# Kernel tuning notes

Hardware: AMD Instinct MI355X
Metric: run time of the kernel (lower is better)

The kernel has to match this reference:

```python
import jax, jax.numpy as jnp
import numpy as np

N = 100000      # nodes
NT = 500000     # unique (s,o) pairs
R = 16          # original relations
RP = 16         # latent relations
EMB = 16
NUMCLS = 40


def setup_inputs() -> dict:
    key = jax.random.key(0)
    ks = jax.random.split(key, 10)
    s = jax.random.randint(ks[0], (NT,), 0, N)
    o = jax.random.randint(ks[1], (NT,), 0, N)
    rm = jnp.arange(RP)
    # faithful to source: oe = o*rm, se = s*rm (values in [0, N*RP))
    hrow = jnp.broadcast_to(s[None, :], (RP, NT)).reshape(-1).astype(jnp.int64)
    hcol = (o[None, :] * rm[:, None]).reshape(-1).astype(jnp.int64)
    vrow = (s[None, :] * rm[:, None]).reshape(-1).astype(jnp.int64)
    vcol = jnp.broadcast_to(o[None, :], (RP, NT)).reshape(-1).astype(jnp.int64)
    # multi-hot relation indicators per unique pair
    nhots = (jax.random.uniform(ks[2], (NT, R)) < 0.15).astype(jnp.float32)
    xav = lambda k, shp, fan: (jax.random.normal(k, shp, jnp.float32) * np.sqrt(2.0 / fan)).astype(jnp.float32)
    return {
        'nhots': nhots,
        'Wl1': xav(ks[3], (RP, R), R), 'bl1': jnp.zeros((RP,), jnp.float32),
        'Wl2': xav(ks[4], (RP, R), R), 'bl2': jnp.zeros((RP,), jnp.float32),
        'weights1': xav(ks[5], (RP, N, EMB), N),
        'weights2': xav(ks[6], (RP, EMB, NUMCLS), EMB),
        'bias1': jnp.zeros((EMB,), jnp.float32),
        'bias2': jnp.zeros((NUMCLS,), jnp.float32),
        'hrow': hrow, 'hcol': hcol, 'vrow': vrow, 'vcol': vcol,
    }


def reference(nhots, Wl1, bl1, Wl2, bl2, weights1, weights2, bias1, bias2,
              hrow, hcol, vrow, vcol):
    rp, n, e = weights1.shape
    nrp = n * rp
    # --- layer 1: softmax-gated latent relation values, column-normalized ---
    lat1 = jax.nn.softmax(nhots @ Wl1.T + bl1, axis=1)          # (nt, rp)
    vals1 = lat1.T.reshape(-1)                                   # (rp*nt,) rp-major, matches index order
    colsum = jax.ops.segment_sum(vals1, hcol, num_segments=nrp)
    vals1 = vals1 / colsum[hcol]
    # spmm: (n, n*rp) sparse  x  (n*rp, e) dense
    wflat = weights1.reshape(nrp, e)
    h = jax.ops.segment_sum(vals1[:, None] * wflat[hcol], hrow, num_segments=n)  # (n, e)
    h = jax.nn.relu(h + bias1)
    # --- layer 2: row-normalized ---
    lat2 = jax.nn.softmax(nhots @ Wl2.T + bl2, axis=1)
    vals2 = lat2.T.reshape(-1)
    rowsum = jax.ops.segment_sum(vals2, vrow, num_segments=nrp)
    vals2 = vals2 / rowsum[vrow]
    # spmm: (n*rp, n) sparse  x  (n, e) dense
    h2 = jax.ops.segment_sum(vals2[:, None] * h[vcol], vrow, num_segments=nrp)   # (n*rp, e)
    h2 = h2.reshape(rp, n, e)
    out = jnp.einsum('rhc,rnh->nc', weights2, h2) + bias2        # (n, numcls)
    return out
```

## Files before the change

### kernel.cpp

```cpp
#include <hip/hip_runtime.h>
#include <stdint.h>

#define NN 100000
#define NT 500000
#define RP 16
#define RR 16
#define EMB 16
#define NUMCLS 40
#define NRP (NN*RP)
#define MM (2*NN)
#define SCAN_BLOCKS ((MM + 255)/256)
#define NB16 6250

__global__ __launch_bounds__(256) void k_count(const int* __restrict__ s,
                                               const int* __restrict__ o,
                                               int* __restrict__ cnt){
    int t = blockIdx.x*256 + threadIdx.x;
    if (t >= NT) return;
    atomicAdd(&cnt[s[t]], 1);
    atomicAdd(&cnt[NN + o[t]], 1);
}

__global__ __launch_bounds__(256) void k_scan_blk(const int* __restrict__ cnt,
                                                  int* __restrict__ offs,
                                                  int* __restrict__ bsum){
    __shared__ int sm[256];
    int tid = threadIdx.x;
    int i = blockIdx.x*256 + tid;
    int v = (i < MM) ? cnt[i] : 0;
    sm[tid] = v; __syncthreads();
    for (int off = 1; off < 256; off <<= 1){
        int x = (tid >= off) ? sm[tid-off] : 0;
        __syncthreads();
        sm[tid] += x; __syncthreads();
    }
    if (i < MM) offs[i] = sm[tid] - v;
    if (tid == 255) bsum[blockIdx.x] = sm[255];
}

__global__ __launch_bounds__(1024) void k_scan_top(const int* __restrict__ bsum,
                                                   int* __restrict__ btot){
    __shared__ int sm[1024];
    int tid = threadIdx.x;
    int v = (tid < SCAN_BLOCKS) ? bsum[tid] : 0;
    sm[tid] = v; __syncthreads();
    for (int off = 1; off < 1024; off <<= 1){
        int x = (tid >= off) ? sm[tid-off] : 0;
        __syncthreads();
        sm[tid] += x; __syncthreads();
    }
    if (tid < SCAN_BLOCKS) btot[tid] = sm[tid] - v;
}

__global__ __launch_bounds__(256) void k_scan_add(int* __restrict__ offs,
                                                  const int* __restrict__ btot,
                                                  int* __restrict__ cur){
    int i = blockIdx.x*256 + threadIdx.x;
    if (i < MM){
        int v = offs[i] + btot[blockIdx.x];
        offs[i] = v;
        cur[i] = v;
    }
    if (i == 0) offs[MM] = 2*NT;
}

__global__ __launch_bounds__(256) void k_lat(
    const float* __restrict__ nhots,
    const float* __restrict__ Wl1, const float* __restrict__ bl1,
    const float* __restrict__ Wl2, const float* __restrict__ bl2,
    const int* __restrict__ srow, const int* __restrict__ ocol,
    int* __restrict__ cur,
    float* __restrict__ lat1q, float* __restrict__ lat2p,
    int* __restrict__ o_at_p, int* __restrict__ s_at_q)
{
    __shared__ float sW1[RP*RR], sW2[RP*RR], sb1[RP], sb2[RP];
    __shared__ float st1[256][17], st2[256][17];
    __shared__ int sq[256], sp[256];
    int tid = threadIdx.x;
    if (tid < RP*RR){ sW1[tid] = Wl1[tid]; sW2[tid] = Wl2[tid]; }
    if (tid < RP){ sb1[tid] = bl1[tid]; sb2[tid] = bl2[tid]; }
    __syncthreads();

    int t = blockIdx.x*256 + tid;
    int p = -1, q = -1;
    if (t < NT){
        int s_ = srow[t], o_ = ocol[t];
        p = atomicAdd(&cur[s_], 1);
        q = atomicAdd(&cur[NN + o_], 1) - NT;
        o_at_p[p] = o_;
        s_at_q[q] = s_;

        float nh[RR];
        const float4* npx = (const float4*)(nhots + (size_t)t * RR);
        #pragma unroll
        for (int u = 0; u < 4; u++){
            float4 v = npx[u];
            nh[4*u] = v.x; nh[4*u+1] = v.y; nh[4*u+2] = v.z; nh[4*u+3] = v.w;
        }
        float l1[RP], l2[RP];
        #pragma unroll
        for (int r = 0; r < RP; r++){
            float a = sb1[r], b = sb2[r];
            #pragma unroll
            for (int i = 0; i < RR; i++){ a += nh[i]*sW1[r*RR+i]; b += nh[i]*sW2[r*RR+i]; }
            l1[r] = a; l2[r] = b;
        }
        float m1 = l1[0], m2 = l2[0];
        #pragma unroll
        for (int r = 1; r < RP; r++){ m1 = fmaxf(m1, l1[r]); m2 = fmaxf(m2, l2[r]); }
        float s1 = 0.f, s2 = 0.f;
        #pragma unroll
        for (int r = 0; r < RP; r++){
            l1[r] = expf(l1[r]-m1); s1 += l1[r];
            l2[r] = expf(l2[r]-m2); s2 += l2[r];
        }
        float i1 = 1.f/s1, i2 = 1.f/s2;
        #pragma unroll
        for (int r = 0; r < RP; r++){ st1[tid][r] = l1[r]*i1; st2[tid][r] = l2[r]*i2; }
    }
    sq[tid] = q; sp[tid] = p;
    __syncthreads();

    int g = tid >> 4, e = tid & 15;
    #pragma unroll
    for (int k = 0; k < 16; k++){
        int ei = k*16 + g;
        int qq = sq[ei];
        if (qq >= 0){
            lat1q[(size_t)qq*16 + e] = st1[ei][e];
            lat2p[(size_t)sp[ei]*16 + e] = st2[ei][e];
        }
    }
}

__global__ __launch_bounds__(256) void k_CR(const int* __restrict__ offs,
                                            const float* __restrict__ lat1q,
                                            const float* __restrict__ lat2p,
                                            float* __restrict__ C,
                                            float* __restrict__ Rm,
                                            float* __restrict__ pbC,
                                            float* __restrict__ pbR){
    int gid = blockIdx.x*256 + threadIdx.x;
    int n = gid >> 4, e = gid & 15;
    float accC = 0.f, accR = 0.f;
    if (n < NN){
        int b = offs[NN+n] - NT, en = offs[NN+n+1] - NT;
        for (int i = b; i < en; i++) accC += lat1q[(size_t)i*16 + e];
        C[(size_t)n*16 + e] = accC;
        b = offs[n]; en = offs[n+1];
        for (int i = b; i < en; i++) accR += lat2p[(size_t)i*16 + e];
        Rm[(size_t)n*16 + e] = accR;
    }
    __shared__ float sa[16], sb[16];
    int g = threadIdx.x >> 4;
    if (e == 0){ sa[g] = accC; sb[g] = accR; }
    __syncthreads();
    if (threadIdx.x == 0){
        float a = 0.f, b = 0.f;
        #pragma unroll
        for (int k = 0; k < 16; k++){ a += sa[k]; b += sb[k]; }
        pbC[blockIdx.x] = a;
        pbR[blockIdx.x] = b;
    }
}

__global__ __launch_bounds__(1024) void k_red1(const float* __restrict__ pbC,
                                               const float* __restrict__ pbR,
                                               float* __restrict__ S0V){
    __shared__ float sa[1024], sb[1024];
    int tid = threadIdx.x;
    float a = 0.f, b = 0.f;
    for (int i = tid; i < NB16; i += 1024){ a += pbC[i]; b += pbR[i]; }
    sa[tid] = a; sb[tid] = b; __syncthreads();
    for (int off = 512; off > 0; off >>= 1){
        if (tid < off){ sa[tid] += sa[tid+off]; sb[tid] += sb[tid+off]; }
        __syncthreads();
    }
    if (tid == 0){ S0V[0] = sa[0]; S0V[1] = sb[0]; }
}

__global__ __launch_bounds__(256) void k_sums(const float* __restrict__ C,
                                              const float* __restrict__ Rm,
                                              const float* __restrict__ S0,
                                              float* __restrict__ invc,
                                              float* __restrict__ invr){
    int c = blockIdx.x*256 + threadIdx.x;
    if (c >= NRP) return;
    float a = 0.f, b = 0.f;
    if (c == 0){ a = S0[0]; b = S0[1]; }
    #pragma unroll
    for (int r = 1; r < RP; r++){
        int q = c / r;
        if (q*r == c && q < NN){
            a += C[(size_t)q*16 + r];
            b += Rm[(size_t)q*16 + r];
        }
    }
    invc[c] = (a > 0.f) ? 1.f/a : 0.f;
    invr[c] = (b > 0.f) ? 1.f/b : 0.f;
}

__global__ __launch_bounds__(256) void k_y(const int* __restrict__ offs,
                                           const float* __restrict__ lat1q,
                                           const int* __restrict__ s_at_q,
                                           const float* __restrict__ invc,
                                           const float* __restrict__ w1,
                                           float* __restrict__ hsum){
    int gid = blockIdx.x*256 + threadIdx.x;
    int o = gid >> 4, e = gid & 15;
    if (o >= NN) return;
    float Wb[RP];
    #pragma unroll
    for (int r = 0; r < RP; r++){
        size_t c = (size_t)o * r;
        Wb[r] = invc[c] * w1[c*16 + e];
    }
    int b = offs[NN+o] - NT, en = offs[NN+o+1] - NT;
    for (int i = b; i < en; i++){
        const float4* lp = (const float4*)(lat1q + (size_t)i*16);
        float4 v0 = lp[0], v1 = lp[1], v2 = lp[2], v3 = lp[3];
        float y = v0.x*Wb[0] + v0.y*Wb[1] + v0.z*Wb[2] + v0.w*Wb[3]
                + v1.x*Wb[4] + v1.y*Wb[5] + v1.z*Wb[6] + v1.w*Wb[7]
                + v2.x*Wb[8] + v2.y*Wb[9] + v2.z*Wb[10]+ v2.w*Wb[11]
                + v3.x*Wb[12]+ v3.y*Wb[13]+ v3.z*Wb[14]+ v3.w*Wb[15];
        int s = s_at_q[i];
        unsafeAtomicAdd(&hsum[(size_t)s*16 + e], y);
    }
}

__global__ __launch_bounds__(256) void k_P(const int* __restrict__ offs,
                                           const int* __restrict__ o_at_p,
                                           const float* __restrict__ lat2p,
                                           const float* __restrict__ hsum,
                                           const float* __restrict__ b1,
                                           float* __restrict__ P,
                                           float* __restrict__ pbV){
    int gid = blockIdx.x*256 + threadIdx.x;
    int n = gid >> 4, e = gid & 15;
    float be = b1[e];
    float acc[RP];
    #pragma unroll
    for (int r = 0; r < RP; r++) acc[r] = 0.f;
    if (n < NN){
        int b = offs[n], en = offs[n+1];
        for (int i = b; i < en; i++){
            int o = o_at_p[i];
            float hv = fmaxf(hsum[(size_t)o*16 + e] + be, 0.f);
            const float4* lp = (const float4*)(lat2p + (size_t)i*16);
            float4 v0 = lp[0], v1 = lp[1], v2 = lp[2], v3 = lp[3];
            acc[0] += v0.x*hv; acc[1] += v0.y*hv; acc[2] += v0.z*hv; acc[3] += v0.w*hv;
            acc[4] += v1.x*hv; acc[5] += v1.y*hv; acc[6] += v1.z*hv; acc[7] += v1.w*hv;
            acc[8] += v2.x*hv; acc[9] += v2.y*hv; acc[10]+= v2.z*hv; acc[11]+= v2.w*hv;
            acc[12]+= v3.x*hv; acc[13]+= v3.y*hv; acc[14]+= v3.z*hv; acc[15]+= v3.w*hv;
        }
        float* Pn = P + (size_t)n*240 + e;
        #pragma unroll
        for (int r = 1; r < RP; r++) Pn[(r-1)*16] = acc[r];
    }
    __shared__ float sm[256];
    sm[threadIdx.x] = acc[0]; __syncthreads();
    if (threadIdx.x < 16){
        float s = 0.f;
        #pragma unroll
        for (int k = 0; k < 16; k++) s += sm[k*16 + threadIdx.x];
        pbV[(size_t)blockIdx.x*16 + threadIdx.x] = s;
    }
}

__global__ __launch_bounds__(256) void k_red2(const float* __restrict__ pbV,
                                              float* __restrict__ S0V){
    int e = blockIdx.x;
    __shared__ float sm[256];
    int tid = threadIdx.x;
    float a = 0.f;
    for (int i = tid; i < NB16; i += 256) a += pbV[(size_t)i*16 + e];
    sm[tid] = a; __syncthreads();
    for (int off = 128; off > 0; off >>= 1){
        if (tid < off) sm[tid] += sm[tid+off];
        __syncthreads();
    }
    if (tid == 0) S0V[2 + e] = sm[0];
}

__global__ __launch_bounds__(256) void k_out(const float* __restrict__ P,
                                             const float* __restrict__ invr,
                                             const float* __restrict__ S0V,
                                             const float* __restrict__ w2,
                                             const float* __restrict__ b2,
                                             float* __restrict__ out){
    __shared__ float sm[4][64][41];
    int tid = threadIdx.x;
    int w = tid >> 6;
    int lane = tid & 63;
    int n = blockIdx.x*64 + lane;
    float acc[NUMCLS];
    #pragma unroll
    for (int cl = 0; cl < NUMCLS; cl++) acc[cl] = 0.f;
    if (n < NN){
        #pragma unroll 1
        for (int rw = 0; rw < 4; rw++){
            int rr = w + rw*4;
            int c = rr*NN + n;
            float hrow[EMB];
            #pragma unroll
            for (int e = 0; e < EMB; e++) hrow[e] = 0.f;
            if (c == 0){
                #pragma unroll
                for (int e = 0; e < EMB; e++) hrow[e] = S0V[2+e];
            }
            #pragma unroll
            for (int r = 1; r < RP; r++){
                int q = c / r;
                if (q*r == c && q < NN){
                    const float4* Pr = (const float4*)(P + (size_t)q*240 + (r-1)*16);
                    float4 a0 = Pr[0], a1 = Pr[1], a2 = Pr[2], a3 = Pr[3];
                    hrow[0]+=a0.x;  hrow[1]+=a0.y;  hrow[2]+=a0.z;  hrow[3]+=a0.w;
                    hrow[4]+=a1.x;  hrow[5]+=a1.y;  hrow[6]+=a1.z;  hrow[7]+=a1.w;
                    hrow[8]+=a2.x;  hrow[9]+=a2.y;  hrow[10]+=a2.z; hrow[11]+=a2.w;
                    hrow[12]+=a3.x; hrow[13]+=a3.y; hrow[14]+=a3.z; hrow[15]+=a3.w;
                }
            }
            float inv = invr[c];
            const float* wr = w2 + (size_t)rr*EMB*NUMCLS;
            #pragma unroll
            for (int e = 0; e < EMB; e++){
                float x = hrow[e] * inv;
                #pragma unroll
                for (int cl = 0; cl < NUMCLS; cl++) acc[cl] += x * wr[e*NUMCLS + cl];
            }
        }
    }
    #pragma unroll
    for (int cl = 0; cl < NUMCLS; cl++) sm[w][lane][cl] = acc[cl];
    __syncthreads();
    int base_n = blockIdx.x*64;
    #pragma unroll
    for (int k = 0; k < 10; k++){
        int f = k*256 + tid;
        int nl = f / 40, cl = f - nl*40;
        int nn = base_n + nl;
        if (nn < NN){
            float v = b2[cl] + sm[0][nl][cl] + sm[1][nl][cl]
                             + sm[2][nl][cl] + sm[3][nl][cl];
            out[(size_t)nn*NUMCLS + cl] = v;
        }
    }
}

extern "C" void kernel_launch(void* const* d_in, const int* in_sizes, int n_in,
                              void* d_out, int out_size, void* d_ws, size_t ws_size,
                              hipStream_t stream)
{
    const float* nhots = (const float*)d_in[0];
    const float* Wl1   = (const float*)d_in[1];
    const float* bl1   = (const float*)d_in[2];
    const float* Wl2   = (const float*)d_in[3];
    const float* bl2   = (const float*)d_in[4];
    const float* w1    = (const float*)d_in[5];
    const float* w2    = (const float*)d_in[6];
    const float* b1    = (const float*)d_in[7];
    const float* b2    = (const float*)d_in[8];
    const int* srow = (const int*)d_in[9];
    const int* ocol = (const int*)d_in[12];

    float* base = (float*)d_ws;
    float* P     = base;
    float* lat1q = base;
    float* C     = base + (size_t)8000000;
    float* Rm    = base + (size_t)9600000;
    float* lat2p = base + (size_t)24000000;
    float* invc  = base + (size_t)32000000;
    float* invr  = base + (size_t)33600000;
    float* hsum  = base + (size_t)35200000;
    float* S0V   = base + (size_t)36800000;
    int*   cnt   = (int*)(base + (size_t)36800032);
    int*   cur   = cnt;
    int*   offs  = cnt + MM;
    int*   bsum  = offs + (MM+1);
    int*   btot  = bsum + 1024;
    int*   o_at_p = btot + 1024;
    int*   s_at_q = o_at_p + NT;
    float* pbC   = (float*)(s_at_q + NT);
    float* pbR   = pbC + NB16;
    float* pbV   = pbR + NB16;

    hipMemsetAsync(cnt, 0, (size_t)MM*4, stream);
    hipMemsetAsync(hsum, 0, (size_t)NN*16*4, stream);

    const int EB = (NT + 255)/256;
    const int CB = (NRP + 255)/256;
    const int OB = (NN + 63)/64;

    k_count   <<<EB, 256, 0, stream>>>(srow, ocol, cnt);
    k_scan_blk<<<SCAN_BLOCKS, 256, 0, stream>>>(cnt, offs, bsum);
    k_scan_top<<<1, 1024, 0, stream>>>(bsum, btot);
    k_scan_add<<<SCAN_BLOCKS, 256, 0, stream>>>(offs, btot, cur);
    k_lat     <<<EB, 256, 0, stream>>>(nhots, Wl1, bl1, Wl2, bl2, srow, ocol,
                                       cur, lat1q, lat2p, o_at_p, s_at_q);
    k_CR      <<<NB16, 256, 0, stream>>>(offs, lat1q, lat2p, C, Rm, pbC, pbR);
    k_red1    <<<1, 1024, 0, stream>>>(pbC, pbR, S0V);
    k_sums    <<<CB, 256, 0, stream>>>(C, Rm, S0V, invc, invr);
    k_y       <<<NB16, 256, 0, stream>>>(offs, lat1q, s_at_q, invc, w1, hsum);
    k_P       <<<NB16, 256, 0, stream>>>(offs, o_at_p, lat2p, hsum, b1, P, pbV);
    k_red2    <<<16, 256, 0, stream>>>(pbV, S0V);
    k_out     <<<OB, 256, 0, stream>>>(P, invr, S0V, w2, b2, (float*)d_out);
}
```

Before: 647.3 us.

## Scatter normalized layer-2 rows with atomics instead of divisor gather in output

k_P now scatters each per-relation partial, pre-scaled by the row normalizer, straight into a dense (NRP,16) h2 buffer with atomic adds, instead of writing a compact P array. k_out then reads the h2 row with one vector load, dropping the 15-way divisibility test and gather loop. This costs a 102 MB memset plus scattered atomics over a larger workspace, and the workspace offsets were shifted to fit it.

```diff
diff --git a/kernel.cpp b/kernel.cpp
--- a/kernel.cpp
+++ b/kernel.cpp
@@ -233,7 +233,8 @@
                                            const float* __restrict__ lat2p,
                                            const float* __restrict__ hsum,
                                            const float* __restrict__ b1,
-                                           float* __restrict__ P,
+                                           const float* __restrict__ invr,
+                                           float* __restrict__ h2n,
                                            float* __restrict__ pbV){
     int gid = blockIdx.x*256 + threadIdx.x;
     int n = gid >> 4, e = gid & 15;
@@ -253,9 +254,11 @@
             acc[8] += v2.x*hv; acc[9] += v2.y*hv; acc[10]+= v2.z*hv; acc[11]+= v2.w*hv;
             acc[12]+= v3.x*hv; acc[13]+= v3.y*hv; acc[14]+= v3.z*hv; acc[15]+= v3.w*hv;
         }
-        float* Pn = P + (size_t)n*240 + e;
-        #pragma unroll
-        for (int r = 1; r < RP; r++) Pn[(r-1)*16] = acc[r];
+        #pragma unroll
+        for (int r = 1; r < RP; r++){
+            size_t c = (size_t)n * r;
+            unsafeAtomicAdd(&h2n[c*16 + e], acc[r] * invr[c]);
+        }
     }
     __shared__ float sm[256];
     sm[threadIdx.x] = acc[0]; __syncthreads();
@@ -282,7 +285,7 @@
     if (tid == 0) S0V[2 + e] = sm[0];
 }
 
-__global__ __launch_bounds__(256) void k_out(const float* __restrict__ P,
+__global__ __launch_bounds__(256) void k_out(const float* __restrict__ h2n,
                                              const float* __restrict__ invr,
                                              const float* __restrict__ S0V,
                                              const float* __restrict__ w2,
@@ -301,30 +304,22 @@
         for (int rw = 0; rw < 4; rw++){
             int rr = w + rw*4;
             int c = rr*NN + n;
-            float hrow[EMB];
-            #pragma unroll
-            for (int e = 0; e < EMB; e++) hrow[e] = 0.f;
+            const float4* hp = (const float4*)(h2n + (size_t)c*16);
+            float4 h0 = hp[0], h1 = hp[1], h2v = hp[2], h3 = hp[3];
+            float hr[EMB];
+            hr[0]=h0.x;  hr[1]=h0.y;  hr[2]=h0.z;  hr[3]=h0.w;
+            hr[4]=h1.x;  hr[5]=h1.y;  hr[6]=h1.z;  hr[7]=h1.w;
+            hr[8]=h2v.x; hr[9]=h2v.y; hr[10]=h2v.z; hr[11]=h2v.w;
+            hr[12]=h3.x; hr[13]=h3.y; hr[14]=h3.z; hr[15]=h3.w;
             if (c == 0){
+                float iv = invr[0];
                 #pragma unroll
-                for (int e = 0; e < EMB; e++) hrow[e] = S0V[2+e];
+                for (int e = 0; e < EMB; e++) hr[e] += S0V[2+e] * iv;
             }
-            #pragma unroll
-            for (int r = 1; r < RP; r++){
-                int q = c / r;
-                if (q*r == c && q < NN){
-                    const float4* Pr = (const float4*)(P + (size_t)q*240 + (r-1)*16);
-                    float4 a0 = Pr[0], a1 = Pr[1], a2 = Pr[2], a3 = Pr[3];
-                    hrow[0]+=a0.x;  hrow[1]+=a0.y;  hrow[2]+=a0.z;  hrow[3]+=a0.w;
-                    hrow[4]+=a1.x;  hrow[5]+=a1.y;  hrow[6]+=a1.z;  hrow[7]+=a1.w;
-                    hrow[8]+=a2.x;  hrow[9]+=a2.y;  hrow[10]+=a2.z; hrow[11]+=a2.w;
-                    hrow[12]+=a3.x; hrow[13]+=a3.y; hrow[14]+=a3.z; hrow[15]+=a3.w;
-                }
-            }
-            float inv = invr[c];
             const float* wr = w2 + (size_t)rr*EMB*NUMCLS;
             #pragma unroll
             for (int e = 0; e < EMB; e++){
-                float x = hrow[e] * inv;
+                float x = hr[e];
                 #pragma unroll
                 for (int cl = 0; cl < NUMCLS; cl++) acc[cl] += x * wr[e*NUMCLS + cl];
             }
@@ -364,16 +359,16 @@
     const int* ocol = (const int*)d_in[12];
 
     float* base = (float*)d_ws;
-    float* P     = base;
+    float* h2n   = base;
     float* lat1q = base;
     float* C     = base + (size_t)8000000;
     float* Rm    = base + (size_t)9600000;
-    float* lat2p = base + (size_t)24000000;
-    float* invc  = base + (size_t)32000000;
-    float* invr  = base + (size_t)33600000;
-    float* hsum  = base + (size_t)35200000;
-    float* S0V   = base + (size_t)36800000;
-    int*   cnt   = (int*)(base + (size_t)36800032);
+    float* lat2p = base + (size_t)25600000;
+    float* invc  = base + (size_t)33600000;
+    float* invr  = base + (size_t)35200000;
+    float* hsum  = base + (size_t)36800000;
+    float* S0V   = base + (size_t)38400000;
+    int*   cnt   = (int*)(base + (size_t)38400032);
     int*   cur   = cnt;
     int*   offs  = cnt + MM;
     int*   bsum  = offs + (MM+1);
@@ -401,7 +396,8 @@
     k_red1    <<<1, 1024, 0, stream>>>(pbC, pbR, S0V);
     k_sums    <<<CB, 256, 0, stream>>>(C, Rm, S0V, invc, invr);
     k_y       <<<NB16, 256, 0, stream>>>(offs, lat1q, s_at_q, invc, w1, hsum);
-    k_P       <<<NB16, 256, 0, stream>>>(offs, o_at_p, lat2p, hsum, b1, P, pbV);
+    hipMemsetAsync(h2n, 0, (size_t)NRP*16*4, stream);
+    k_P       <<<NB16, 256, 0, stream>>>(offs, o_at_p, lat2p, hsum, b1, invr, h2n, pbV);
     k_red2    <<<16, 256, 0, stream>>>(pbV, S0V);
-    k_out     <<<OB, 256, 0, stream>>>(P, invr, S0V, w2, b2, (float*)d_out);
-}
+    k_out     <<<OB, 256, 0, stream>>>(h2n, invr, S0V, w2, b2, (float*)d_out);
+}
```

New measurement: 686.4 us. 6.0% more time.
